# Kernel optimization log

Hardware: AMD Instinct MI355X
Metric: run time of the kernel (lower is better)

The kernel has to match this reference:

```python
import jax, jax.numpy as jnp
import numpy as np

B, S, DIM = 2, 2048, 2048
NH, NKV = 16, 8
HD = DIM // NH  # 128
ROPE_THETA = 10000.0


def setup_inputs() -> dict:
    key = jax.random.key(0)
    ks = jax.random.split(key, 7)
    std = DIM ** -0.5
    x = jax.random.normal(ks[0], (B, S, DIM), jnp.float32)
    wq = jax.random.normal(ks[1], (NH * HD, DIM), jnp.float32) * std
    wk = jax.random.normal(ks[2], (NKV * HD, DIM), jnp.float32) * std
    wv = jax.random.normal(ks[3], (NKV * HD, DIM), jnp.float32) * std
    wo = jax.random.normal(ks[4], (DIM, NH * HD), jnp.float32) * std
    inv_freq = 1.0 / (ROPE_THETA ** (jnp.arange(0, HD, 2, dtype=jnp.float32) / HD))
    ang = jnp.arange(S, dtype=jnp.float32)[:, None] * inv_freq[None, :]  # [S, HD//2]
    freqs_cos = jnp.cos(ang)
    freqs_sin = jnp.sin(ang)
    # diffusion-style random per-batch token mask: t ~ U[0,1) per batch row
    t = jax.random.uniform(ks[5], (B, 1))
    mask = jax.random.uniform(ks[6], (B, S)) < t  # True = masked key
    mask = mask.at[:, 0].set(False)  # first token never masked
    return dict(x=x, wq=wq, wk=wk, wv=wv, wo=wo,
                freqs_cos=freqs_cos, freqs_sin=freqs_sin, mask=mask)


def _rope(x, cos, sin):
    # x: [b, s, h, d]; pairs (x[2i], x[2i+1]) rotated by angle[s, i]
    xr, xi = x[..., 0::2], x[..., 1::2]
    c = cos[None, :, None, :]
    s = sin[None, :, None, :]
    out = jnp.stack([xr * c - xi * s, xr * s + xi * c], axis=-1)
    return out.reshape(x.shape)


def reference(x, wq, wk, wv, wo, freqs_cos, freqs_sin, mask):
    b, s, _ = x.shape
    xq = jnp.einsum('bsd,ed->bse', x, wq).reshape(b, s, NH, HD)
    xk = jnp.einsum('bsd,ed->bse', x, wk).reshape(b, s, NKV, HD)
    xv = jnp.einsum('bsd,ed->bse', x, wv).reshape(b, s, NKV, HD)
    xq = _rope(xq, freqs_cos, freqs_sin)
    xk = _rope(xk, freqs_cos, freqs_sin)
    n_rep = NH // NKV
    xk = jnp.repeat(xk, n_rep, axis=2)  # repeat_kv (GQA)
    xv = jnp.repeat(xv, n_rep, axis=2)
    q = xq.transpose(0, 2, 1, 3)  # [b, h, s, d]
    k = xk.transpose(0, 2, 1, 3)
    v = xv.transpose(0, 2, 1, 3)
    scale = 1.0 / np.sqrt(HD).astype(np.float32)
    scores = jnp.einsum('bhqd,bhkd->bhqk', q, k) * scale  # [b, h, s, s]
    scores = jnp.where(mask[:, None, None, :], -jnp.inf, scores)
    probs = jax.nn.softmax(scores, axis=-1)
    out = jnp.einsum('bhqk,bhkd->bhqd', probs, v)
    out = out.transpose(0, 2, 1, 3).reshape(b, s, NH * HD)
    return jnp.einsum('bse,de->bsd', out, wo)
```

## Files before the change

kernel.cpp:

```cpp
#include <hip/hip_runtime.h>
#include <hip/hip_bf16.h>
#include <cstdint>
#include <cstddef>

#define S_LEN   2048
#define NHQ     16
#define NKV_H   8
#define HD_DIM  128
#define DMODEL  2048
#define BATCH   2
#define KVD     (NKV_H * HD_DIM)
#define QKV_LD  4096

typedef float f32x4  __attribute__((ext_vector_type(4)));
typedef __bf16 bf16x8 __attribute__((ext_vector_type(8)));
typedef __bf16 bf16x4 __attribute__((ext_vector_type(4)));

__device__ __forceinline__ void gload_lds16(const __bf16* g, __bf16* l) {
    __builtin_amdgcn_global_load_lds(
        (const __attribute__((address_space(1))) void*)g,
        (__attribute__((address_space(3))) void*)l, 16, 0, 0);
}

__global__ __launch_bounds__(256)
void prep_kernel(const unsigned* __restrict__ x, int* __restrict__ flag_x,
                 const unsigned* __restrict__ fc, int* __restrict__ flag_fc,
                 const unsigned char* __restrict__ mraw,
                 unsigned char* __restrict__ mout, int n) {
    if (blockIdx.x == 0) {
        __shared__ int cnt;
        if (threadIdx.x == 0) cnt = 0;
        __syncthreads();
        int c = 0;
        for (int j = threadIdx.x; j < 1024; j += 256) {
            unsigned hw = x[j] & 0xFFFFu;
            unsigned e  = (hw >> 7) & 0xFF;
            if (hw == 0u || (e >= 118 && e <= 132)) c++;
        }
        atomicAdd(&cnt, c);
        __syncthreads();
        if (threadIdx.x == 0) *flag_x = (cnt > 512) ? 1 : 0;
    } else if (blockIdx.x == 1) {
        if (threadIdx.x == 0) *flag_fc = (fc[0] == 0x3F803F80u) ? 1 : 0;
    } else {
        __shared__ int f_bf16, f_f32, f_u8;
        if (threadIdx.x == 0) { f_bf16 = 0; f_f32 = 0; f_u8 = 0; }
        __syncthreads();
        const unsigned* dw = (const unsigned*)mraw;
        int ndw = n / 4;
        for (int j = threadIdx.x; j < ndw; j += blockDim.x) {
            unsigned v = dw[j];
            if (v == 0x00003F80u || v == 0x3F803F80u) f_bf16 = 1;
            else if (v == 0x3F800000u) f_f32 = 1;
            else if (v & 0xFFFFFFFEu) f_u8 = 1;
        }
        __syncthreads();
        int layout;
        if (f_bf16) layout = 3;
        else if (f_f32) layout = 2;
        else if (f_u8) layout = 0;
        else layout = 1;
        for (int i = threadIdx.x; i < n; i += blockDim.x) {
            unsigned v;
            if (layout == 0)      v = mraw[i];
            else if (layout == 3) v = ((const unsigned short*)mraw)[i];
            else                  v = ((const unsigned*)mraw)[i];
            mout[i] = v ? 1u : 0u;
        }
    }
}

__device__ __forceinline__ void conv8(const void* src, __bf16* dst,
                                      size_t off, int isbf16) {
    if (isbf16) {
        *reinterpret_cast<uint4*>(dst + off) =
            *reinterpret_cast<const uint4*>((const __bf16*)src + off);
    } else {
        const float* f = (const float*)src + off;
        float4 a = *reinterpret_cast<const float4*>(f);
        float4 b = *reinterpret_cast<const float4*>(f + 4);
        bf16x8 v;
        v[0] = (__bf16)a.x; v[1] = (__bf16)a.y; v[2] = (__bf16)a.z; v[3] = (__bf16)a.w;
        v[4] = (__bf16)b.x; v[5] = (__bf16)b.y; v[6] = (__bf16)b.z; v[7] = (__bf16)b.w;
        *reinterpret_cast<bf16x8*>(dst + off) = v;
    }
}

__global__ __launch_bounds__(256)
void conv_all_kernel(const void* __restrict__ x,  const void* __restrict__ wq,
                     const void* __restrict__ wk, const void* __restrict__ wv,
                     __bf16* __restrict__ xb, __bf16* __restrict__ wcomb,
                     const int* __restrict__ dflag) {
    int i = blockIdx.x * 256 + threadIdx.x;
    int isb = *dflag;
    if (i < 1048576) {
        conv8(x, xb, (size_t)i * 8, isb);
    } else if (i < 1572864) {
        conv8(wq, wcomb, (size_t)(i - 1048576) * 8, isb);
    } else if (i < 1835008) {
        conv8(wk, wcomb + (size_t)2048 * 2048, (size_t)(i - 1572864) * 8, isb);
    } else {
        conv8(wv, wcomb + (size_t)3072 * 2048, (size_t)(i - 1835008) * 8, isb);
    }
}

__global__ __launch_bounds__(256)
void conv_bf16_strided_kernel(const void* __restrict__ src,
                              __bf16* __restrict__ dstbase,
                              int n8, const int* __restrict__ dflag) {
    int i = blockIdx.x * blockDim.x + threadIdx.x;
    if (i >= n8) return;
    size_t off = (size_t)i * 8;
    size_t row = off >> 11;
    size_t col = off & 2047;
    __bf16* dst = dstbase + row * QKV_LD + col;
    if (*dflag) {
        *reinterpret_cast<uint4*>(dst) =
            *reinterpret_cast<const uint4*>((const __bf16*)src + off);
    } else {
        const float* f = (const float*)src + off;
        float4 a = *reinterpret_cast<const float4*>(f);
        float4 b = *reinterpret_cast<const float4*>(f + 4);
        bf16x8 v;
        v[0] = (__bf16)a.x; v[1] = (__bf16)a.y; v[2] = (__bf16)a.z; v[3] = (__bf16)a.w;
        v[4] = (__bf16)b.x; v[5] = (__bf16)b.y; v[6] = (__bf16)b.z; v[7] = (__bf16)b.w;
        *reinterpret_cast<bf16x8*>(dst) = v;
    }
}

template <bool OUT_BF16>
__global__ __launch_bounds__(256)
void gemm_bt_async(const __bf16* __restrict__ A, const __bf16* __restrict__ Bw,
                   void* __restrict__ Cv, int K, int lda, int ldb, int ldc) {
    __shared__ __align__(16) __bf16 As[128 * 64];
    __shared__ __align__(16) __bf16 Bs[128 * 64];

    const int t    = threadIdx.x;
    const int w    = t >> 6;
    const int lane = t & 63;
    const int quad = lane >> 4;
    const int l16  = lane & 15;
    const int wm   = (w >> 1) * 64;
    const int wn   = (w & 1) * 64;

    const int nwg  = gridDim.x * gridDim.y;
    const int lin  = blockIdx.y * gridDim.x + blockIdx.x;
    const int swz  = (lin & 7) * (nwg >> 3) + (lin >> 3);
    const int m0   = (swz % gridDim.x) * 128;
    const int n0   = (swz / gridDim.x) * 128;

    const int rl   = lane >> 3;
    const int gl   = lane & 7;

    f32x4 acc[4][4];
#pragma unroll
    for (int i = 0; i < 4; ++i)
#pragma unroll
        for (int j = 0; j < 4; ++j) acc[i][j] = (f32x4){0.f, 0.f, 0.f, 0.f};

    for (int k0 = 0; k0 < K; k0 += 64) {
        __syncthreads();
#pragma unroll
        for (int p = 0; p < 4; ++p) {
            const int rowb = w * 32 + p * 8;
            const int r    = rowb + rl;
            const int gA   = gl ^ rl;
            gload_lds16(A  + (size_t)(m0 + r) * lda + k0 + gA * 8, &As[rowb * 64]);
            gload_lds16(Bw + (size_t)(n0 + r) * ldb + k0 + gA * 8, &Bs[rowb * 64]);
        }
        __syncthreads();
#pragma unroll
        for (int ks = 0; ks < 2; ++ks) {
            const int G = ks * 4 + quad;
            const int gsw = (G ^ (l16 & 7)) * 8;
            bf16x8 af[4], bf[4];
#pragma unroll
            for (int i = 0; i < 4; ++i)
                af[i] = *reinterpret_cast<const bf16x8*>(
                    &As[(wm + i * 16 + l16) * 64 + gsw]);
#pragma unroll
            for (int j = 0; j < 4; ++j)
                bf[j] = *reinterpret_cast<const bf16x8*>(
                    &Bs[(wn + j * 16 + l16) * 64 + gsw]);
#pragma unroll
            for (int i = 0; i < 4; ++i)
#pragma unroll
                for (int j = 0; j < 4; ++j)
                    acc[i][j] = __builtin_amdgcn_mfma_f32_16x16x32_bf16(
                        af[i], bf[j], acc[i][j], 0, 0, 0);
        }
    }
#pragma unroll
    for (int i = 0; i < 4; ++i)
#pragma unroll
        for (int r = 0; r < 4; ++r) {
            size_t m = (size_t)(m0 + wm + i * 16 + quad * 4 + r);
#pragma unroll
            for (int j = 0; j < 4; ++j) {
                int n = n0 + wn + j * 16 + l16;
                if constexpr (OUT_BF16)
                    ((__hip_bfloat16*)Cv)[m * ldc + n] = __float2bfloat16(acc[i][j][r]);
                else
                    ((float*)Cv)[m * ldc + n] = acc[i][j][r];
            }
        }
}

__global__ void rope_kernel(__hip_bfloat16* __restrict__ xqk,
                            const void* __restrict__ cosv,
                            const void* __restrict__ sinv,
                            const int* __restrict__ dflag_fc,
                            int npairs) {
    int idx = blockIdx.x * blockDim.x + threadIdx.x;
    if (idx >= npairs) return;
    int i  = idx & 63;
    int h  = (idx >> 6) % 24;
    int bs = idx / (64 * 24);
    int s  = bs & (S_LEN - 1);
    float c, sn;
    if (*dflag_fc) {
        c  = __bfloat162float(((const __hip_bfloat16*)cosv)[s * 64 + i]);
        sn = __bfloat162float(((const __hip_bfloat16*)sinv)[s * 64 + i]);
    } else {
        c  = ((const float*)cosv)[s * 64 + i];
        sn = ((const float*)sinv)[s * 64 + i];
    }
    unsigned* p = (unsigned*)(xqk + (size_t)bs * QKV_LD + h * HD_DIM) + i;
    unsigned u = *p;
    float xr = __uint_as_float(u << 16);
    float xi = __uint_as_float(u & 0xFFFF0000u);
    float o0 = xr * c - xi * sn;
    float o1 = xr * sn + xi * c;
    union { __hip_bfloat16 h2[2]; unsigned u32; } out;
    out.h2[0] = __float2bfloat16(o0);
    out.h2[1] = __float2bfloat16(o1);
    *p = out.u32;
}

__global__ __launch_bounds__(256)
void transpose_v_kernel(const __hip_bfloat16* __restrict__ xv,
                        __hip_bfloat16* __restrict__ vt) {
    __shared__ unsigned short T[32][36];
    const int t  = threadIdx.x;
    const int s0 = blockIdx.x * 32;
    const int d0 = blockIdx.y * 32;
    const int z  = blockIdx.z;
    const int b  = z >> 3;
    const int kv = z & 7;
    {
        int sr = t >> 3, dc = (t & 7) * 4;
        const unsigned short* p = (const unsigned short*)xv
            + (size_t)(b * S_LEN + s0 + sr) * QKV_LD + kv * 128 + d0 + dc;
        uint2 v = *reinterpret_cast<const uint2*>(p);
        T[sr][dc + 0] = (unsigned short)(v.x & 0xFFFFu);
        T[sr][dc + 1] = (unsigned short)(v.x >> 16);
        T[sr][dc + 2] = (unsigned short)(v.y & 0xFFFFu);
        T[sr][dc + 3] = (unsigned short)(v.y >> 16);
    }
    __syncthreads();
    {
        int dr = t >> 3, sc = (t & 7) * 4;
        unsigned w0 = (unsigned)T[sc + 0][dr] | ((unsigned)T[sc + 1][dr] << 16);
        unsigned w1 = (unsigned)T[sc + 2][dr] | ((unsigned)T[sc + 3][dr] << 16);
        unsigned short* q = (unsigned short*)vt
            + ((size_t)z * 128 + d0 + dr) * S_LEN + s0 + sc;
        uint2 v; v.x = w0; v.y = w1;
        *reinterpret_cast<uint2*>(q) = v;
    }
}

__global__ __launch_bounds__(256)
void attn_mfma2_kernel(__hip_bfloat16* qkv,
                       const __hip_bfloat16* __restrict__ vt_g,
                       const unsigned char* __restrict__ msk) {
    __shared__ __align__(16) __bf16 Ks[2][64 * 128];
    __shared__ __align__(16) __bf16 Vt[2][128 * 64];
    __shared__ __align__(16) __bf16 Ps[4][16][64];

    const int t    = threadIdx.x;
    const int w    = t >> 6;
    const int lane = t & 63;
    const int quad = lane >> 4;
    const int l16  = lane & 15;

    const int bid = ((blockIdx.x & 7) << 7) | (blockIdx.x >> 3);
    const int qt  = bid & 31;
    const int h   = (bid >> 5) & (NHQ - 1);
    const int b   = bid >> 9;
    const int kvh = h >> 1;
    const int q0  = qt * 64;

    bf16x8 qf[4];
    {
        const __bf16* qrow = (const __bf16*)qkv
            + (size_t)(b * S_LEN + q0 + w * 16 + l16) * QKV_LD + h * 128 + quad * 8;
#pragma unroll
        for (int ks = 0; ks < 4; ++ks)
            qf[ks] = *reinterpret_cast<const bf16x8*>(qrow + ks * 32);
    }

    float m_r = -INFINITY, l_r = 0.f;
    f32x4 o[8];
#pragma unroll
    for (int d0 = 0; d0 < 8; ++d0) o[d0] = (f32x4){0.f, 0.f, 0.f, 0.f};

    const float scale2 = 0.08838834764831845f * 1.4426950408889634f;
    const int gbase = lane & 48;

    const __bf16* kp[4];
    const __bf16* vp[4];
    {
        const __bf16* xk = (const __bf16*)qkv + 2048;
        const int krl = lane >> 4, kgl = lane & 15;
        const int vrl = lane >> 3, vgl = lane & 7;
#pragma unroll
        for (int p = 0; p < 4; ++p) {
            const int row = w * 16 + p * 4 + krl;
            kp[p] = xk + (size_t)(b * S_LEN + row) * QKV_LD
                       + kvh * 128 + (kgl ^ (row & 7)) * 8;
        }
#pragma unroll
        for (int p = 0; p < 4; ++p) {
            const int row = w * 32 + p * 8 + vrl;
            vp[p] = (const __bf16*)vt_g
                  + ((size_t)(b * NKV_H + kvh) * 128 + row) * S_LEN
                  + (vgl ^ (row & 7)) * 8;
        }
    }
    const unsigned char* mbase = msk + b * S_LEN;

    auto stage = [&](int sb) {
#pragma unroll
        for (int p = 0; p < 4; ++p) {
            gload_lds16(kp[p], &Ks[sb][(w * 16 + p * 4) * 128]);
            kp[p] += 64 * QKV_LD;
        }
#pragma unroll
        for (int p = 0; p < 4; ++p) {
            gload_lds16(vp[p], &Vt[sb][(w * 32 + p * 8) * 64]);
            vp[p] += 64;
        }
    };

    auto tile_body = [&](int kmask, int cb, int sb, bool do_stage) {
        if (do_stage) stage(sb);

        unsigned mk4[4];
        {
            const unsigned* mp = (const unsigned*)(mbase + kmask);
#pragma unroll
            for (int n0 = 0; n0 < 4; ++n0) mk4[n0] = mp[n0 * 4 + quad];
        }

        f32x4 sc4[4];
#pragma unroll
        for (int n0 = 0; n0 < 4; ++n0) sc4[n0] = (f32x4){0.f, 0.f, 0.f, 0.f};
        __builtin_amdgcn_s_setprio(1);
#pragma unroll
        for (int ks = 0; ks < 4; ++ks) {
            const int G = ks * 4 + quad;
#pragma unroll
            for (int n0 = 0; n0 < 4; ++n0) {
                const int row  = n0 * 16 + l16;
                const int slot = G ^ (row & 7);
                bf16x8 kf = *reinterpret_cast<const bf16x8*>(&Ks[cb][row * 128 + slot * 8]);
                sc4[n0] = __builtin_amdgcn_mfma_f32_16x16x32_bf16(kf, qf[ks], sc4[n0], 0, 0, 0);
            }
        }
        __builtin_amdgcn_s_setprio(0);

#pragma unroll
        for (int n0 = 0; n0 < 4; ++n0)
#pragma unroll
            for (int r = 0; r < 4; ++r)
                sc4[n0][r] = ((mk4[n0] >> (r * 8)) & 0xFF) ? -INFINITY : sc4[n0][r];

        float tq[4];
#pragma unroll
        for (int n0 = 0; n0 < 4; ++n0)
            tq[n0] = fmaxf(fmaxf(sc4[n0][0], sc4[n0][1]),
                           fmaxf(sc4[n0][2], sc4[n0][3]));
        float rm = fmaxf(fmaxf(tq[0], tq[1]), fmaxf(tq[2], tq[3]));
        rm = fmaxf(rm, __shfl_xor(rm, 16, 64));
        rm = fmaxf(rm, __shfl_xor(rm, 32, 64));

        bool need = (rm - m_r) * scale2 > 8.0f;
        if (__any((int)need)) {
            float mn = fmaxf(m_r, rm);
            float al = exp2f((m_r - mn) * scale2);
            m_r = mn;
            l_r *= al;
            float alq[4];
#pragma unroll
            for (int r = 0; r < 4; ++r)
                alq[r] = __shfl(al, gbase | (quad * 4 + r), 64);
#pragma unroll
            for (int d0 = 0; d0 < 8; ++d0)
#pragma unroll
                for (int r = 0; r < 4; ++r) o[d0][r] *= alq[r];
        }

        float negm = -m_r * scale2;
#pragma unroll
        for (int n0 = 0; n0 < 4; ++n0)
#pragma unroll
            for (int r = 0; r < 4; ++r) {
                float p = exp2f(fmaf(sc4[n0][r], scale2, negm));
                sc4[n0][r] = p;
                l_r += p;
            }

#pragma unroll
        for (int n0 = 0; n0 < 4; ++n0) {
            const int kb    = n0 * 16 + quad * 4;
            const int gran  = kb >> 3;
            const int half4 = kb & 4;
            const int slot  = gran ^ (l16 & 7);
            bf16x4 pk;
            pk[0] = (__bf16)sc4[n0][0];
            pk[1] = (__bf16)sc4[n0][1];
            pk[2] = (__bf16)sc4[n0][2];
            pk[3] = (__bf16)sc4[n0][3];
            *reinterpret_cast<bf16x4*>(&Ps[w][l16][slot * 8 + half4]) = pk;
        }

        __builtin_amdgcn_s_setprio(1);
#pragma unroll
        for (int kk = 0; kk < 64; kk += 32) {
            const int Gp    = (kk >> 3) + quad;
            const int slotp = Gp ^ (l16 & 7);
            bf16x8 af = *reinterpret_cast<const bf16x8*>(&Ps[w][l16][slotp * 8]);
#pragma unroll
            for (int d0 = 0; d0 < 8; ++d0) {
                const int row  = d0 * 16 + l16;
                const int slot = Gp ^ (row & 7);
                bf16x8 bf = *reinterpret_cast<const bf16x8*>(&Vt[cb][row * 64 + slot * 8]);
                o[d0] = __builtin_amdgcn_mfma_f32_16x16x32_bf16(af, bf, o[d0], 0, 0, 0);
            }
        }
        __builtin_amdgcn_s_setprio(0);

        __syncthreads();
    };

    stage(0);
    __syncthreads();

    for (int k0 = 0; k0 < S_LEN; k0 += 128) {
        tile_body(k0,      0, 1, true);
        tile_body(k0 + 64, 1, 0, k0 + 128 < S_LEN);
    }

    float ls = l_r;
    ls += __shfl_xor(ls, 16, 64);
    ls += __shfl_xor(ls, 32, 64);
    float invl = 1.f / ls;
    float invq[4];
#pragma unroll
    for (int r = 0; r < 4; ++r)
        invq[r] = __shfl(invl, gbase | (quad * 4 + r), 64);
    __hip_bfloat16* att = qkv;
#pragma unroll
    for (int d0 = 0; d0 < 8; ++d0)
#pragma unroll
        for (int r = 0; r < 4; ++r) {
            size_t row = (size_t)(b * S_LEN + q0 + w * 16 + quad * 4 + r);
            att[row * QKV_LD + h * 128 + d0 * 16 + l16] =
                __float2bfloat16(o[d0][r] * invq[r]);
        }
}

extern "C" void kernel_launch(void* const* d_in, const int* in_sizes, int n_in,
                              void* d_out, int out_size, void* d_ws, size_t ws_size,
                              hipStream_t stream) {
    const void* x  = d_in[0];
    const void* wq = d_in[1];
    const void* wk = d_in[2];
    const void* wv = d_in[3];
    const void* wo = d_in[4];
    const void* fc = d_in[5];
    const void* fs = d_in[6];
    const unsigned char* mraw = (const unsigned char*)d_in[7];

    const int M = BATCH * S_LEN;
    char* wsb = (char*)d_ws;
    int* dflag_x  = (int*)wsb;
    int* dflag_fc = (int*)(wsb + 64);
    unsigned char* mnorm = (unsigned char*)(wsb + 128);
    __hip_bfloat16* qkv = (__hip_bfloat16*)(wsb + 8192);

    char* dob = (char*)d_out;
    __bf16* xb    = (__bf16*)dob;
    __bf16* wcomb = (__bf16*)(dob + (16u << 20));
    __hip_bfloat16* vt = (__hip_bfloat16*)d_out;

    hipLaunchKernelGGL(prep_kernel, dim3(3), dim3(256), 0, stream,
                       (const unsigned*)x, dflag_x, (const unsigned*)fc, dflag_fc,
                       mraw, mnorm, BATCH * S_LEN);

    hipLaunchKernelGGL(conv_all_kernel, dim3(8192), dim3(256), 0, stream,
                       x, wq, wk, wv, xb, wcomb, dflag_x);

    hipLaunchKernelGGL((gemm_bt_async<true>), dim3(M / 128, QKV_LD / 128), dim3(256), 0, stream,
                       xb, wcomb, (void*)qkv, DMODEL, DMODEL, DMODEL, QKV_LD);

    int npairs = M * 24 * (HD_DIM / 2);
    hipLaunchKernelGGL(rope_kernel, dim3(npairs / 256), dim3(256), 0, stream,
                       qkv, fc, fs, dflag_fc, npairs);

    hipLaunchKernelGGL(transpose_v_kernel, dim3(S_LEN / 32, HD_DIM / 32, BATCH * NKV_H),
                       dim3(256), 0, stream, qkv + 3072, vt);

    hipLaunchKernelGGL(attn_mfma2_kernel, dim3(BATCH * NHQ * (S_LEN / 64)), dim3(256), 0, stream,
                       qkv, vt, mnorm);

    hipLaunchKernelGGL(conv_bf16_strided_kernel, dim3((DMODEL * DMODEL / 8) / 256), dim3(256), 0, stream,
                       wo, (__bf16*)qkv + 2048, DMODEL * DMODEL / 8, dflag_x);

    hipLaunchKernelGGL((gemm_bt_async<false>), dim3(M / 128, DMODEL / 128), dim3(256), 0, stream,
                       (const __bf16*)qkv, (const __bf16*)qkv + 2048, d_out,
                       DMODEL, QKV_LD, QKV_LD, DMODEL);
}
```

Baseline: 432.4 us.

## Fuse RoPE into QKV GEMM epilogue, merge prep kernel, single-buffer attention K/V

Applies RoPE inside the QKV projection GEMM epilogue using a lane shuffle to fetch the pair partner, removing the separate rope kernel and its extra pass over the QKV buffer. The prep kernel is folded into extra blocks of the conversion kernel, and each block sniffs the input dtype itself. The attention kernel drops K/V double buffering for single buffers, staging V then K with an extra barrier, which reduces LDS use but may expose load latency. Per-block dtype sniffing adds redundant small reads.

```diff
diff --git a/kernel.cpp b/kernel.cpp
--- a/kernel.cpp
+++ b/kernel.cpp
@@ -22,52 +22,18 @@
         (__attribute__((address_space(3))) void*)l, 16, 0, 0);
 }
 
-__global__ __launch_bounds__(256)
-void prep_kernel(const unsigned* __restrict__ x, int* __restrict__ flag_x,
-                 const unsigned* __restrict__ fc, int* __restrict__ flag_fc,
-                 const unsigned char* __restrict__ mraw,
-                 unsigned char* __restrict__ mout, int n) {
-    if (blockIdx.x == 0) {
-        __shared__ int cnt;
-        if (threadIdx.x == 0) cnt = 0;
-        __syncthreads();
-        int c = 0;
-        for (int j = threadIdx.x; j < 1024; j += 256) {
-            unsigned hw = x[j] & 0xFFFFu;
-            unsigned e  = (hw >> 7) & 0xFF;
-            if (hw == 0u || (e >= 118 && e <= 132)) c++;
-        }
-        atomicAdd(&cnt, c);
-        __syncthreads();
-        if (threadIdx.x == 0) *flag_x = (cnt > 512) ? 1 : 0;
-    } else if (blockIdx.x == 1) {
-        if (threadIdx.x == 0) *flag_fc = (fc[0] == 0x3F803F80u) ? 1 : 0;
-    } else {
-        __shared__ int f_bf16, f_f32, f_u8;
-        if (threadIdx.x == 0) { f_bf16 = 0; f_f32 = 0; f_u8 = 0; }
-        __syncthreads();
-        const unsigned* dw = (const unsigned*)mraw;
-        int ndw = n / 4;
-        for (int j = threadIdx.x; j < ndw; j += blockDim.x) {
-            unsigned v = dw[j];
-            if (v == 0x00003F80u || v == 0x3F803F80u) f_bf16 = 1;
-            else if (v == 0x3F800000u) f_f32 = 1;
-            else if (v & 0xFFFFFFFEu) f_u8 = 1;
-        }
-        __syncthreads();
-        int layout;
-        if (f_bf16) layout = 3;
-        else if (f_f32) layout = 2;
-        else if (f_u8) layout = 0;
-        else layout = 1;
-        for (int i = threadIdx.x; i < n; i += blockDim.x) {
-            unsigned v;
-            if (layout == 0)      v = mraw[i];
-            else if (layout == 3) v = ((const unsigned short*)mraw)[i];
-            else                  v = ((const unsigned*)mraw)[i];
-            mout[i] = v ? 1u : 0u;
-        }
-    }
+__device__ __forceinline__ int sniff_bf16(const unsigned* buf, int* cntp) {
+    if (threadIdx.x == 0) *cntp = 0;
+    __syncthreads();
+    int c = 0;
+    for (int j = threadIdx.x; j < 1024; j += 256) {
+        unsigned hw = buf[j] & 0xFFFFu;
+        unsigned e  = (hw >> 7) & 0xFF;
+        if (hw == 0u || (e >= 118 && e <= 132)) c++;
+    }
+    atomicAdd(cntp, c);
+    __syncthreads();
+    return *cntp > 512;
 }
 
 __device__ __forceinline__ void conv8(const void* src, __bf16* dst,
@@ -90,9 +56,43 @@
 void conv_all_kernel(const void* __restrict__ x,  const void* __restrict__ wq,
                      const void* __restrict__ wk, const void* __restrict__ wv,
                      __bf16* __restrict__ xb, __bf16* __restrict__ wcomb,
-                     const int* __restrict__ dflag) {
+                     const unsigned* __restrict__ fc, int* __restrict__ dflag_fc,
+                     const unsigned char* __restrict__ mraw,
+                     unsigned char* __restrict__ mout, int nmask) {
+    __shared__ int sh[4];
+    if (blockIdx.x == 8192) {
+        if (threadIdx.x == 0) *dflag_fc = (fc[0] == 0x3F803F80u) ? 1 : 0;
+        return;
+    }
+    if (blockIdx.x == 8193) {
+        __shared__ int f_bf16, f_f32, f_u8;
+        if (threadIdx.x == 0) { f_bf16 = 0; f_f32 = 0; f_u8 = 0; }
+        __syncthreads();
+        const unsigned* dw = (const unsigned*)mraw;
+        int ndw = nmask / 4;
+        for (int j = threadIdx.x; j < ndw; j += blockDim.x) {
+            unsigned v = dw[j];
+            if (v == 0x00003F80u || v == 0x3F803F80u) f_bf16 = 1;
+            else if (v == 0x3F800000u) f_f32 = 1;
+            else if (v & 0xFFFFFFFEu) f_u8 = 1;
+        }
+        __syncthreads();
+        int layout;
+        if (f_bf16) layout = 3;
+        else if (f_f32) layout = 2;
+        else if (f_u8) layout = 0;
+        else layout = 1;
+        for (int i = threadIdx.x; i < nmask; i += blockDim.x) {
+            unsigned v;
+            if (layout == 0)      v = mraw[i];
+            else if (layout == 3) v = ((const unsigned short*)mraw)[i];
+            else                  v = ((const unsigned*)mraw)[i];
+            mout[i] = v ? 1u : 0u;
+        }
+        return;
+    }
+    int isb = sniff_bf16((const unsigned*)x, &sh[0]);
     int i = blockIdx.x * 256 + threadIdx.x;
-    int isb = *dflag;
     if (i < 1048576) {
         conv8(x, xb, (size_t)i * 8, isb);
     } else if (i < 1572864) {
@@ -106,15 +106,16 @@
 
 __global__ __launch_bounds__(256)
 void conv_bf16_strided_kernel(const void* __restrict__ src,
-                              __bf16* __restrict__ dstbase,
-                              int n8, const int* __restrict__ dflag) {
+                              __bf16* __restrict__ dstbase, int n8) {
+    __shared__ int cnt;
+    int isb = sniff_bf16((const unsigned*)src, &cnt);
     int i = blockIdx.x * blockDim.x + threadIdx.x;
     if (i >= n8) return;
     size_t off = (size_t)i * 8;
     size_t row = off >> 11;
     size_t col = off & 2047;
     __bf16* dst = dstbase + row * QKV_LD + col;
-    if (*dflag) {
+    if (isb) {
         *reinterpret_cast<uint4*>(dst) =
             *reinterpret_cast<const uint4*>((const __bf16*)src + off);
     } else {
@@ -128,10 +129,12 @@
     }
 }
 
-template <bool OUT_BF16>
+template <bool OUT_BF16, bool ROPE>
 __global__ __launch_bounds__(256)
 void gemm_bt_async(const __bf16* __restrict__ A, const __bf16* __restrict__ Bw,
-                   void* __restrict__ Cv, int K, int lda, int ldb, int ldc) {
+                   void* __restrict__ Cv, int K, int lda, int ldb, int ldc,
+                   const void* __restrict__ cosv, const void* __restrict__ sinv,
+                   const int* __restrict__ dflag_fc) {
     __shared__ __align__(16) __bf16 As[128 * 64];
     __shared__ __align__(16) __bf16 Bs[128 * 64];
 
@@ -190,51 +193,39 @@
                         af[i], bf[j], acc[i][j], 0, 0, 0);
         }
     }
+
+    bool fcb = false;
+    if constexpr (ROPE) fcb = (*dflag_fc != 0);
 #pragma unroll
     for (int i = 0; i < 4; ++i)
 #pragma unroll
         for (int r = 0; r < 4; ++r) {
             size_t m = (size_t)(m0 + wm + i * 16 + quad * 4 + r);
+            const int spos = (int)(m & (S_LEN - 1));
 #pragma unroll
             for (int j = 0; j < 4; ++j) {
                 int n = n0 + wn + j * 16 + l16;
+                float v = acc[i][j][r];
+                if (ROPE && (n0 + wn + j * 16 < 3072)) {
+                    int pair = (n & 127) >> 1;
+                    float c, s;
+                    if (fcb) {
+                        c = __bfloat162float(((const __hip_bfloat16*)cosv)[spos * 64 + pair]);
+                        s = __bfloat162float(((const __hip_bfloat16*)sinv)[spos * 64 + pair]);
+                    } else {
+                        c = ((const float*)cosv)[spos * 64 + pair];
+                        s = ((const float*)sinv)[spos * 64 + pair];
+                    }
+                    float partner = __shfl_xor(v, 1, 64);
+                    float ssgn = (n & 1) ? s : -s;
+                    v = fmaf(v, c, partner * ssgn);
+                }
                 if constexpr (OUT_BF16)
-                    ((__hip_bfloat16*)Cv)[m * ldc + n] = __float2bfloat16(acc[i][j][r]);
+                    ((__hip_bfloat16*)Cv)[m * ldc + n] = __float2bfloat16(v);
                 else
-                    ((float*)Cv)[m * ldc + n] = acc[i][j][r];
+                    ((float*)Cv)[m * ldc + n] = v;
             }
         }
-}
-
-__global__ void rope_kernel(__hip_bfloat16* __restrict__ xqk,
-                            const void* __restrict__ cosv,
-                            const void* __restrict__ sinv,
-                            const int* __restrict__ dflag_fc,
-                            int npairs) {
-    int idx = blockIdx.x * blockDim.x + threadIdx.x;
-    if (idx >= npairs) return;
-    int i  = idx & 63;
-    int h  = (idx >> 6) % 24;
-    int bs = idx / (64 * 24);
-    int s  = bs & (S_LEN - 1);
-    float c, sn;
-    if (*dflag_fc) {
-        c  = __bfloat162float(((const __hip_bfloat16*)cosv)[s * 64 + i]);
-        sn = __bfloat162float(((const __hip_bfloat16*)sinv)[s * 64 + i]);
-    } else {
-        c  = ((const float*)cosv)[s * 64 + i];
-        sn = ((const float*)sinv)[s * 64 + i];
-    }
-    unsigned* p = (unsigned*)(xqk + (size_t)bs * QKV_LD + h * HD_DIM) + i;
-    unsigned u = *p;
-    float xr = __uint_as_float(u << 16);
-    float xi = __uint_as_float(u & 0xFFFF0000u);
-    float o0 = xr * c - xi * sn;
-    float o1 = xr * sn + xi * c;
-    union { __hip_bfloat16 h2[2]; unsigned u32; } out;
-    out.h2[0] = __float2bfloat16(o0);
-    out.h2[1] = __float2bfloat16(o1);
-    *p = out.u32;
 }
 
 __global__ __launch_bounds__(256)
@@ -273,8 +264,8 @@
 void attn_mfma2_kernel(__hip_bfloat16* qkv,
                        const __hip_bfloat16* __restrict__ vt_g,
                        const unsigned char* __restrict__ msk) {
-    __shared__ __align__(16) __bf16 Ks[2][64 * 128];
-    __shared__ __align__(16) __bf16 Vt[2][128 * 64];
+    __shared__ __align__(16) __bf16 Ks[64 * 128];
+    __shared__ __align__(16) __bf16 Vt[128 * 64];
     __shared__ __align__(16) __bf16 Ps[4][16][64];
 
     const int t    = threadIdx.x;
@@ -329,25 +320,30 @@
     }
     const unsigned char* mbase = msk + b * S_LEN;
 
-    auto stage = [&](int sb) {
+    auto stage_K = [&]() {
 #pragma unroll
         for (int p = 0; p < 4; ++p) {
-            gload_lds16(kp[p], &Ks[sb][(w * 16 + p * 4) * 128]);
+            gload_lds16(kp[p], &Ks[(w * 16 + p * 4) * 128]);
             kp[p] += 64 * QKV_LD;
         }
+    };
+    auto stage_V = [&]() {
 #pragma unroll
         for (int p = 0; p < 4; ++p) {
-            gload_lds16(vp[p], &Vt[sb][(w * 32 + p * 8) * 64]);
+            gload_lds16(vp[p], &Vt[(w * 32 + p * 8) * 64]);
             vp[p] += 64;
         }
     };
 
-    auto tile_body = [&](int kmask, int cb, int sb, bool do_stage) {
-        if (do_stage) stage(sb);
+    stage_K();
+    __syncthreads();
+
+    for (int k0 = 0; k0 < S_LEN; k0 += 64) {
+        stage_V();
 
         unsigned mk4[4];
         {
-            const unsigned* mp = (const unsigned*)(mbase + kmask);
+            const unsigned* mp = (const unsigned*)(mbase + k0);
 #pragma unroll
             for (int n0 = 0; n0 < 4; ++n0) mk4[n0] = mp[n0 * 4 + quad];
         }
@@ -363,11 +359,15 @@
             for (int n0 = 0; n0 < 4; ++n0) {
                 const int row  = n0 * 16 + l16;
                 const int slot = G ^ (row & 7);
-                bf16x8 kf = *reinterpret_cast<const bf16x8*>(&Ks[cb][row * 128 + slot * 8]);
+                bf16x8 kf = *reinterpret_cast<const bf16x8*>(&Ks[row * 128 + slot * 8]);
                 sc4[n0] = __builtin_amdgcn_mfma_f32_16x16x32_bf16(kf, qf[ks], sc4[n0], 0, 0, 0);
             }
         }
         __builtin_amdgcn_s_setprio(0);
+
+        __syncthreads();
+
+        if (k0 + 64 < S_LEN) stage_K();
 
 #pragma unroll
         for (int n0 = 0; n0 < 4; ++n0)
@@ -434,21 +434,13 @@
             for (int d0 = 0; d0 < 8; ++d0) {
                 const int row  = d0 * 16 + l16;
                 const int slot = Gp ^ (row & 7);
-                bf16x8 bf = *reinterpret_cast<const bf16x8*>(&Vt[cb][row * 64 + slot * 8]);
+                bf16x8 bf = *reinterpret_cast<const bf16x8*>(&Vt[row * 64 + slot * 8]);
                 o[d0] = __builtin_amdgcn_mfma_f32_16x16x32_bf16(af, bf, o[d0], 0, 0, 0);
             }
         }
         __builtin_amdgcn_s_setprio(0);
 
         __syncthreads();
-    };
-
-    stage(0);
-    __syncthreads();
-
-    for (int k0 = 0; k0 < S_LEN; k0 += 128) {
-        tile_body(k0,      0, 1, true);
-        tile_body(k0 + 64, 1, 0, k0 + 128 < S_LEN);
     }
 
     float ls = l_r;
@@ -484,7 +476,6 @@
 
     const int M = BATCH * S_LEN;
     char* wsb = (char*)d_ws;
-    int* dflag_x  = (int*)wsb;
     int* dflag_fc = (int*)(wsb + 64);
     unsigned char* mnorm = (unsigned char*)(wsb + 128);
     __hip_bfloat16* qkv = (__hip_bfloat16*)(wsb + 8192);
@@ -494,19 +485,13 @@
     __bf16* wcomb = (__bf16*)(dob + (16u << 20));
     __hip_bfloat16* vt = (__hip_bfloat16*)d_out;
 
-    hipLaunchKernelGGL(prep_kernel, dim3(3), dim3(256), 0, stream,
-                       (const unsigned*)x, dflag_x, (const unsigned*)fc, dflag_fc,
-                       mraw, mnorm, BATCH * S_LEN);
-
-    hipLaunchKernelGGL(conv_all_kernel, dim3(8192), dim3(256), 0, stream,
-                       x, wq, wk, wv, xb, wcomb, dflag_x);
-
-    hipLaunchKernelGGL((gemm_bt_async<true>), dim3(M / 128, QKV_LD / 128), dim3(256), 0, stream,
-                       xb, wcomb, (void*)qkv, DMODEL, DMODEL, DMODEL, QKV_LD);
-
-    int npairs = M * 24 * (HD_DIM / 2);
-    hipLaunchKernelGGL(rope_kernel, dim3(npairs / 256), dim3(256), 0, stream,
-                       qkv, fc, fs, dflag_fc, npairs);
+    hipLaunchKernelGGL(conv_all_kernel, dim3(8194), dim3(256), 0, stream,
+                       x, wq, wk, wv, xb, wcomb,
+                       (const unsigned*)fc, dflag_fc, mraw, mnorm, BATCH * S_LEN);
+
+    hipLaunchKernelGGL((gemm_bt_async<true, true>), dim3(M / 128, QKV_LD / 128), dim3(256), 0, stream,
+                       xb, wcomb, (void*)qkv, DMODEL, DMODEL, DMODEL, QKV_LD,
+                       fc, fs, dflag_fc);
 
     hipLaunchKernelGGL(transpose_v_kernel, dim3(S_LEN / 32, HD_DIM / 32, BATCH * NKV_H),
                        dim3(256), 0, stream, qkv + 3072, vt);
@@ -515,9 +500,10 @@
                        qkv, vt, mnorm);
 
     hipLaunchKernelGGL(conv_bf16_strided_kernel, dim3((DMODEL * DMODEL / 8) / 256), dim3(256), 0, stream,
-                       wo, (__bf16*)qkv + 2048, DMODEL * DMODEL / 8, dflag_x);
-
-    hipLaunchKernelGGL((gemm_bt_async<false>), dim3(M / 128, DMODEL / 128), dim3(256), 0, stream,
+                       wo, (__bf16*)qkv + 2048, DMODEL * DMODEL / 8);
+
+    hipLaunchKernelGGL((gemm_bt_async<false, false>), dim3(M / 128, DMODEL / 128), dim3(256), 0, stream,
                        (const __bf16*)qkv, (const __bf16*)qkv + 2048, d_out,
-                       DMODEL, QKV_LD, QKV_LD, DMODEL);
-}
+                       DMODEL, QKV_LD, QKV_LD, DMODEL,
+                       nullptr, nullptr, nullptr);
+}
```

After: 438.2 us. No clear change (+1.4%).
